# Kernel optimization log

Hardware: AMD Instinct MI355X
Metric: run time of the kernel (lower is better)

The kernel has to match this reference:

```python
import jax, jax.numpy as jnp
import numpy as np

N_NODES = 50000
N_EDGES = 500000
D_NODE = 128
D_EDGE = 128
D_HID = 512
D_OUT = 128


def setup_inputs() -> dict:
    key = jax.random.key(0)
    ks = jax.random.split(key, 6)
    x = jax.random.normal(ks[0], (N_NODES, D_NODE), dtype=jnp.float32)
    edge_index = jax.random.randint(ks[1], (2, N_EDGES), 0, N_NODES, dtype=jnp.int64 if jax.config.jax_enable_x64 else jnp.int32)
    edge_attr = jax.random.normal(ks[2], (N_EDGES, D_EDGE), dtype=jnp.float32)
    cin = 2 * D_NODE + D_EDGE
    W1 = jax.random.normal(ks[3], (cin, D_HID), dtype=jnp.float32) * (1.0 / np.sqrt(cin))
    b1 = jnp.zeros((D_HID,), dtype=jnp.float32)
    W2 = jax.random.normal(ks[4], (D_HID, D_OUT), dtype=jnp.float32) * (1.0 / np.sqrt(D_HID))
    b2 = jnp.zeros((D_OUT,), dtype=jnp.float32)
    return {"x": x, "edge_index": edge_index, "edge_attr": edge_attr,
            "W1": W1, "b1": b1, "W2": W2, "b2": b2}


def reference(x, edge_index, edge_attr, W1, b1, W2, b2):
    row, col = edge_index[0], edge_index[1]
    source = x[row]            # [E, d_node] gather
    target = x[col]            # [E, d_node] gather
    out = jnp.concatenate([source, target, edge_attr], axis=1)  # [E, 2*d_node + d_edge]
    h = jax.nn.relu(out @ W1 + b1)   # [E, d_hid]
    return h @ W2 + b2               # [E, d_out]
```

## Files before the change

kernel.cpp:

```cpp
#include <hip/hip_runtime.h>

#define E_TOTAL 500000
#define DN 128
#define CIN 384
#define DH 512
#define DOUT 128
#define MT 64
#define NBLK 7813
#define LDA 392
#define LDH 520

typedef short short8 __attribute__((ext_vector_type(8)));
typedef float f32x4 __attribute__((ext_vector_type(4)));

__device__ inline short f2bf(float f) {
    unsigned int u = __float_as_uint(f);
    u = (u + 0x7FFFu + ((u >> 16) & 1u)) >> 16;
    return (short)u;
}

__global__ void prep_weights(const float* __restrict__ w1,
                             const float* __restrict__ w2,
                             short* __restrict__ w1t,
                             short* __restrict__ w2t) {
    __shared__ float t[32][33];
    int b = blockIdx.x;
    const float* src; short* dst; int R, C, tr, tc;
    if (b < 192) { src = w1; dst = w1t; R = 384; C = 512; tr = b >> 4; tc = b & 15; }
    else { b -= 192; src = w2; dst = w2t; R = 512; C = 128; tr = b >> 2; tc = b & 3; }
    int lx = threadIdx.x & 31, ly = threadIdx.x >> 5;
#pragma unroll
    for (int p = 0; p < 4; p++) {
        int r = tr * 32 + p * 8 + ly;
        t[p * 8 + ly][lx] = src[(size_t)r * C + tc * 32 + lx];
    }
    __syncthreads();
#pragma unroll
    for (int p = 0; p < 4; p++) {
        int c = tc * 32 + p * 8 + ly;
        dst[(size_t)c * R + tr * 32 + lx] = f2bf(t[lx][p * 8 + ly]);
    }
}

__global__ __launch_bounds__(512, 4) void edge_mlp(
        const float* __restrict__ x,
        const int* __restrict__ ei,
        const float* __restrict__ ea,
        const float* __restrict__ b1,
        const float* __restrict__ b2,
        const short* __restrict__ w1t,
        const short* __restrict__ w2t,
        float* __restrict__ out) {
    __shared__ short sBuf[MT * LDH];
    __shared__ int sIdx[2][MT];
    short (*sA)[LDA] = (short (*)[LDA])sBuf;
    short (*sH)[LDH] = (short (*)[LDH])sBuf;

    const int tid = threadIdx.x;
    const int wave = tid >> 6;
    const int lane = tid & 63;
    const int l16 = lane & 15;
    const int quad = lane >> 4;
    const int e0 = blockIdx.x * MT;

    if (tid < MT) {
        int e = e0 + tid; e = e < E_TOTAL ? e : E_TOTAL - 1;
        sIdx[0][tid] = ei[e];
    } else if (tid < 2 * MT) {
        int r = tid - MT;
        int e = e0 + r; e = e < E_TOTAL ? e : E_TOTAL - 1;
        sIdx[1][r] = ei[E_TOTAL + e];
    }
    __syncthreads();

    {
        const int lane32 = tid & 31;
        const int g = tid >> 5;
        for (int u = g; u < 3 * MT; u += 16) {
            int seg = u >> 6;
            int r = u & 63;
            const float* src;
            if (seg == 0)      src = x + (size_t)sIdx[0][r] * DN;
            else if (seg == 1) src = x + (size_t)sIdx[1][r] * DN;
            else {
                int e = e0 + r; e = e < E_TOTAL ? e : E_TOTAL - 1;
                src = ea + (size_t)e * DN;
            }
            float4 v = reinterpret_cast<const float4*>(src)[lane32];
            short4 p;
            p.x = f2bf(v.x); p.y = f2bf(v.y); p.z = f2bf(v.z); p.w = f2bf(v.w);
            *reinterpret_cast<short4*>(&sA[r][seg * DN + lane32 * 4]) = p;
        }
    }
    __syncthreads();

    f32x4 acc[4][4] = {};
    {
        const int nb = wave * 64;
        const short* base = w1t + (size_t)(nb + l16) * CIN + quad * 8;
        short8 bb[4];
#pragma unroll
        for (int nt = 0; nt < 4; nt++)
            bb[nt] = *reinterpret_cast<const short8*>(base + nt * 16 * CIN);
        for (int k = 0; k < CIN; k += 32) {
            short8 bn[4];
            if (k + 32 < CIN) {
#pragma unroll
                for (int nt = 0; nt < 4; nt++)
                    bn[nt] = *reinterpret_cast<const short8*>(base + nt * 16 * CIN + k + 32);
            }
            short8 a[4];
#pragma unroll
            for (int mt = 0; mt < 4; mt++)
                a[mt] = *reinterpret_cast<const short8*>(&sA[mt * 16 + l16][k + quad * 8]);
#pragma unroll
            for (int nt = 0; nt < 4; nt++)
#pragma unroll
                for (int mt = 0; mt < 4; mt++)
                    acc[mt][nt] = __builtin_amdgcn_mfma_f32_16x16x32_bf16(a[mt], bb[nt], acc[mt][nt], 0, 0, 0);
            if (k + 32 < CIN) {
#pragma unroll
                for (int nt = 0; nt < 4; nt++) bb[nt] = bn[nt];
            }
        }
        __syncthreads();
#pragma unroll
        for (int nt = 0; nt < 4; nt++) {
            int n = nb + nt * 16 + l16;
            float bias = b1[n];
#pragma unroll
            for (int mt = 0; mt < 4; mt++)
#pragma unroll
                for (int r = 0; r < 4; r++) {
                    int m = mt * 16 + quad * 4 + r;
                    sH[m][n] = f2bf(fmaxf(acc[mt][nt][r] + bias, 0.0f));
                }
        }
    }
    __syncthreads();

    {
        f32x4 acc2[4] = {};
        const int n = wave * 16 + l16;
        const short* base2 = w2t + (size_t)n * DH + quad * 8;
        short8 bb = *reinterpret_cast<const short8*>(base2);
        for (int k = 0; k < DH; k += 32) {
            short8 bn;
            if (k + 32 < DH)
                bn = *reinterpret_cast<const short8*>(base2 + k + 32);
            short8 h[4];
#pragma unroll
            for (int mt = 0; mt < 4; mt++)
                h[mt] = *reinterpret_cast<const short8*>(&sH[mt * 16 + l16][k + quad * 8]);
#pragma unroll
            for (int mt = 0; mt < 4; mt++)
                acc2[mt] = __builtin_amdgcn_mfma_f32_16x16x32_bf16(h[mt], bb, acc2[mt], 0, 0, 0);
            if (k + 32 < DH) bb = bn;
        }
        float bias = b2[n];
#pragma unroll
        for (int mt = 0; mt < 4; mt++)
#pragma unroll
            for (int r = 0; r < 4; r++) {
                int m = mt * 16 + quad * 4 + r;
                int e = e0 + m;
                if (e < E_TOTAL)
                    out[(size_t)e * DOUT + n] = acc2[mt][r] + bias;
            }
    }
}

extern "C" void kernel_launch(void* const* d_in, const int* in_sizes, int n_in,
                              void* d_out, int out_size, void* d_ws, size_t ws_size,
                              hipStream_t stream) {
    const float* x  = (const float*)d_in[0];
    const int*   ei = (const int*)d_in[1];
    const float* ea = (const float*)d_in[2];
    const float* W1 = (const float*)d_in[3];
    const float* b1 = (const float*)d_in[4];
    const float* W2 = (const float*)d_in[5];
    const float* b2 = (const float*)d_in[6];
    float* outp = (float*)d_out;

    short* w1t = (short*)d_ws;
    short* w2t = w1t + DH * CIN;

    prep_weights<<<256, 256, 0, stream>>>(W1, W2, w1t, w2t);
    edge_mlp<<<NBLK, 512, 0, stream>>>(x, ei, ea, b1, b2, w1t, w2t, outp);
}
```

Measured before the change: 972.7 us.

## Make edge MLP persistent with software-pipelined gather of next tile

Turns the per-tile grid into 512 persistent blocks that loop over tiles with a stride. The next tile's node and edge features are loaded into registers during the first GEMM epilogue and the second GEMM, and the indices two tiles ahead are prefetched. The MFMA operands are swapped so each lane holds four consecutive columns, which allows vectorized short4 stores to the hidden buffer and float4 output stores. This is meant to hide gather latency behind compute and cut launch overhead, at the cost of more registers per thread and possibly lower occupancy.

```diff
diff --git a/kernel.cpp b/kernel.cpp
--- a/kernel.cpp
+++ b/kernel.cpp
@@ -6,7 +6,8 @@
 #define DH 512
 #define DOUT 128
 #define MT 64
-#define NBLK 7813
+#define NTILE 7813
+#define NPERS 512
 #define LDA 392
 #define LDH 520
 
@@ -52,7 +53,7 @@
         const short* __restrict__ w2t,
         float* __restrict__ out) {
     __shared__ short sBuf[MT * LDH];
-    __shared__ int sIdx[2][MT];
+    __shared__ int sIdx[2][2][MT];
     short (*sA)[LDA] = (short (*)[LDA])sBuf;
     short (*sH)[LDH] = (short (*)[LDH])sBuf;
 
@@ -61,112 +62,172 @@
     const int lane = tid & 63;
     const int l16 = lane & 15;
     const int quad = lane >> 4;
-    const int e0 = blockIdx.x * MT;
-
-    if (tid < MT) {
-        int e = e0 + tid; e = e < E_TOTAL ? e : E_TOTAL - 1;
-        sIdx[0][tid] = ei[e];
-    } else if (tid < 2 * MT) {
-        int r = tid - MT;
-        int e = e0 + r; e = e < E_TOTAL ? e : E_TOTAL - 1;
-        sIdx[1][r] = ei[E_TOTAL + e];
+    const int lane32 = tid & 31;
+    const int g = tid >> 5;
+    const int t0 = blockIdx.x;
+
+    float4 b1v[4];
+#pragma unroll
+    for (int nt = 0; nt < 4; nt++)
+        b1v[nt] = *reinterpret_cast<const float4*>(&b1[wave * 64 + nt * 16 + quad * 4]);
+    float4 b2v = *reinterpret_cast<const float4*>(&b2[wave * 16 + quad * 4]);
+
+    if (tid < 2 * MT) {
+        int rrow = tid >> 6, r = tid & 63;
+        int e = t0 * MT + r; e = e < E_TOTAL ? e : E_TOTAL - 1;
+        sIdx[0][rrow][r] = ei[rrow * E_TOTAL + e];
+        if (t0 + NPERS < NTILE) {
+            int e2 = (t0 + NPERS) * MT + r; e2 = e2 < E_TOTAL ? e2 : E_TOTAL - 1;
+            sIdx[1][rrow][r] = ei[rrow * E_TOTAL + e2];
+        }
     }
     __syncthreads();
-
-    {
-        const int lane32 = tid & 31;
-        const int g = tid >> 5;
-        for (int u = g; u < 3 * MT; u += 16) {
-            int seg = u >> 6;
-            int r = u & 63;
-            const float* src;
-            if (seg == 0)      src = x + (size_t)sIdx[0][r] * DN;
-            else if (seg == 1) src = x + (size_t)sIdx[1][r] * DN;
-            else {
-                int e = e0 + r; e = e < E_TOTAL ? e : E_TOTAL - 1;
-                src = ea + (size_t)e * DN;
-            }
-            float4 v = reinterpret_cast<const float4*>(src)[lane32];
+#pragma unroll
+    for (int j = 0; j < 12; j++) {
+        const int seg = j >> 2;
+        const int r = g + 16 * (j & 3);
+        const float* src;
+        if (seg == 0)      src = x + (size_t)sIdx[0][0][r] * DN;
+        else if (seg == 1) src = x + (size_t)sIdx[0][1][r] * DN;
+        else { int e = t0 * MT + r; e = e < E_TOTAL ? e : E_TOTAL - 1; src = ea + (size_t)e * DN; }
+        float4 v = reinterpret_cast<const float4*>(src)[lane32];
+        short4 p; p.x = f2bf(v.x); p.y = f2bf(v.y); p.z = f2bf(v.z); p.w = f2bf(v.w);
+        *reinterpret_cast<short4*>(&sA[r][seg * DN + lane32 * 4]) = p;
+    }
+    __syncthreads();
+
+#pragma unroll 1
+    for (int i = 0; ; i++) {
+        const int t = t0 + i * NPERS;
+        const int e0 = t * MT;
+        const bool hasN1 = (t + NPERS) < NTILE;
+        const bool hasN2 = (t + 2 * NPERS) < NTILE;
+
+        f32x4 acc[4][4] = {};
+        {
+            const short* base1 = w1t + (size_t)(wave * 64 + l16) * CIN + quad * 8;
+            short8 bb[4];
+#pragma unroll
+            for (int nt = 0; nt < 4; nt++)
+                bb[nt] = *reinterpret_cast<const short8*>(base1 + nt * 16 * CIN);
+            for (int k = 0; k < CIN; k += 32) {
+                short8 bn[4];
+                if (k + 32 < CIN) {
+#pragma unroll
+                    for (int nt = 0; nt < 4; nt++)
+                        bn[nt] = *reinterpret_cast<const short8*>(base1 + nt * 16 * CIN + k + 32);
+                }
+                short8 a[4];
+#pragma unroll
+                for (int mt = 0; mt < 4; mt++)
+                    a[mt] = *reinterpret_cast<const short8*>(&sA[mt * 16 + l16][k + quad * 8]);
+#pragma unroll
+                for (int nt = 0; nt < 4; nt++)
+#pragma unroll
+                    for (int mt = 0; mt < 4; mt++)
+                        acc[nt][mt] = __builtin_amdgcn_mfma_f32_16x16x32_bf16(bb[nt], a[mt], acc[nt][mt], 0, 0, 0);
+                if (k + 32 < CIN) {
+#pragma unroll
+                    for (int nt = 0; nt < 4; nt++) bb[nt] = bn[nt];
+                }
+            }
+        }
+        asm volatile("s_waitcnt lgkmcnt(0)" ::: "memory");
+        __builtin_amdgcn_s_barrier();
+
+#pragma unroll
+        for (int nt = 0; nt < 4; nt++) {
+#pragma unroll
+            for (int mt = 0; mt < 4; mt++) {
+                short4 p;
+                p.x = f2bf(fmaxf(acc[nt][mt][0] + b1v[nt].x, 0.0f));
+                p.y = f2bf(fmaxf(acc[nt][mt][1] + b1v[nt].y, 0.0f));
+                p.z = f2bf(fmaxf(acc[nt][mt][2] + b1v[nt].z, 0.0f));
+                p.w = f2bf(fmaxf(acc[nt][mt][3] + b1v[nt].w, 0.0f));
+                *reinterpret_cast<short4*>(&sH[mt * 16 + l16][wave * 64 + nt * 16 + quad * 4]) = p;
+            }
+        }
+
+        const short* base2 = w2t + (size_t)(wave * 16 + l16) * DH + quad * 8;
+        short8 b2f[4];
+#pragma unroll
+        for (int kk = 0; kk < 4; kk++)
+            b2f[kk] = *reinterpret_cast<const short8*>(base2 + kk * 32);
+
+        float4 gv[12];
+        if (hasN1) {
+            const int* sI0 = sIdx[(i + 1) & 1][0];
+            const int* sI1 = sIdx[(i + 1) & 1][1];
+            const int e0n = (t + NPERS) * MT;
+#pragma unroll
+            for (int j = 0; j < 12; j++) {
+                const int seg = j >> 2;
+                const int r = g + 16 * (j & 3);
+                const float* src;
+                if (seg == 0)      src = x + (size_t)sI0[r] * DN;
+                else if (seg == 1) src = x + (size_t)sI1[r] * DN;
+                else { int e = e0n + r; e = e < E_TOTAL ? e : E_TOTAL - 1; src = ea + (size_t)e * DN; }
+                gv[j] = reinterpret_cast<const float4*>(src)[lane32];
+            }
+        }
+        int idxN = 0;
+        if (hasN2 && tid < 2 * MT) {
+            int rrow = tid >> 6, r = tid & 63;
+            int e2 = (t + 2 * NPERS) * MT + r; e2 = e2 < E_TOTAL ? e2 : E_TOTAL - 1;
+            idxN = ei[rrow * E_TOTAL + e2];
+        }
+        __builtin_amdgcn_sched_barrier(0);
+        asm volatile("s_waitcnt lgkmcnt(0)" ::: "memory");
+        __builtin_amdgcn_s_barrier();
+
+        {
+            f32x4 acc2[4] = {};
+            short8 bw = b2f[0];
+#pragma unroll
+            for (int kk = 0; kk < 16; kk++) {
+                short8 bnext = bw;
+                if (kk < 3) bnext = b2f[kk + 1];
+                else if (kk < 15) bnext = *reinterpret_cast<const short8*>(base2 + (kk + 1) * 32);
+                short8 h[4];
+#pragma unroll
+                for (int mt = 0; mt < 4; mt++)
+                    h[mt] = *reinterpret_cast<const short8*>(&sH[mt * 16 + l16][kk * 32 + quad * 8]);
+#pragma unroll
+                for (int mt = 0; mt < 4; mt++)
+                    acc2[mt] = __builtin_amdgcn_mfma_f32_16x16x32_bf16(bw, h[mt], acc2[mt], 0, 0, 0);
+                bw = bnext;
+            }
+#pragma unroll
+            for (int mt = 0; mt < 4; mt++) {
+                int e = e0 + mt * 16 + l16;
+                if (e < E_TOTAL) {
+                    float4 o;
+                    o.x = acc2[mt][0] + b2v.x;
+                    o.y = acc2[mt][1] + b2v.y;
+                    o.z = acc2[mt][2] + b2v.z;
+                    o.w = acc2[mt][3] + b2v.w;
+                    *reinterpret_cast<float4*>(&out[(size_t)e * DOUT + wave * 16 + quad * 4]) = o;
+                }
+            }
+        }
+
+        if (!hasN1) break;
+
+        asm volatile("s_waitcnt lgkmcnt(0)" ::: "memory");
+        __builtin_amdgcn_s_barrier();
+
+#pragma unroll
+        for (int j = 0; j < 12; j++) {
+            const int seg = j >> 2;
+            const int r = g + 16 * (j & 3);
             short4 p;
-            p.x = f2bf(v.x); p.y = f2bf(v.y); p.z = f2bf(v.z); p.w = f2bf(v.w);
+            p.x = f2bf(gv[j].x); p.y = f2bf(gv[j].y); p.z = f2bf(gv[j].z); p.w = f2bf(gv[j].w);
             *reinterpret_cast<short4*>(&sA[r][seg * DN + lane32 * 4]) = p;
         }
-    }
-    __syncthreads();
-
-    f32x4 acc[4][4] = {};
-    {
-        const int nb = wave * 64;
-        const short* base = w1t + (size_t)(nb + l16) * CIN + quad * 8;
-        short8 bb[4];
-#pragma unroll
-        for (int nt = 0; nt < 4; nt++)
-            bb[nt] = *reinterpret_cast<const short8*>(base + nt * 16 * CIN);
-        for (int k = 0; k < CIN; k += 32) {
-            short8 bn[4];
-            if (k + 32 < CIN) {
-#pragma unroll
-                for (int nt = 0; nt < 4; nt++)
-                    bn[nt] = *reinterpret_cast<const short8*>(base + nt * 16 * CIN + k + 32);
-            }
-            short8 a[4];
-#pragma unroll
-            for (int mt = 0; mt < 4; mt++)
-                a[mt] = *reinterpret_cast<const short8*>(&sA[mt * 16 + l16][k + quad * 8]);
-#pragma unroll
-            for (int nt = 0; nt < 4; nt++)
-#pragma unroll
-                for (int mt = 0; mt < 4; mt++)
-                    acc[mt][nt] = __builtin_amdgcn_mfma_f32_16x16x32_bf16(a[mt], bb[nt], acc[mt][nt], 0, 0, 0);
-            if (k + 32 < CIN) {
-#pragma unroll
-                for (int nt = 0; nt < 4; nt++) bb[nt] = bn[nt];
-            }
-        }
-        __syncthreads();
-#pragma unroll
-        for (int nt = 0; nt < 4; nt++) {
-            int n = nb + nt * 16 + l16;
-            float bias = b1[n];
-#pragma unroll
-            for (int mt = 0; mt < 4; mt++)
-#pragma unroll
-                for (int r = 0; r < 4; r++) {
-                    int m = mt * 16 + quad * 4 + r;
-                    sH[m][n] = f2bf(fmaxf(acc[mt][nt][r] + bias, 0.0f));
-                }
-        }
-    }
-    __syncthreads();
-
-    {
-        f32x4 acc2[4] = {};
-        const int n = wave * 16 + l16;
-        const short* base2 = w2t + (size_t)n * DH + quad * 8;
-        short8 bb = *reinterpret_cast<const short8*>(base2);
-        for (int k = 0; k < DH; k += 32) {
-            short8 bn;
-            if (k + 32 < DH)
-                bn = *reinterpret_cast<const short8*>(base2 + k + 32);
-            short8 h[4];
-#pragma unroll
-            for (int mt = 0; mt < 4; mt++)
-                h[mt] = *reinterpret_cast<const short8*>(&sH[mt * 16 + l16][k + quad * 8]);
-#pragma unroll
-            for (int mt = 0; mt < 4; mt++)
-                acc2[mt] = __builtin_amdgcn_mfma_f32_16x16x32_bf16(h[mt], bb, acc2[mt], 0, 0, 0);
-            if (k + 32 < DH) bb = bn;
-        }
-        float bias = b2[n];
-#pragma unroll
-        for (int mt = 0; mt < 4; mt++)
-#pragma unroll
-            for (int r = 0; r < 4; r++) {
-                int m = mt * 16 + quad * 4 + r;
-                int e = e0 + m;
-                if (e < E_TOTAL)
-                    out[(size_t)e * DOUT + n] = acc2[mt][r] + bias;
-            }
+        if (hasN2 && tid < 2 * MT)
+            sIdx[i & 1][tid >> 6][tid & 63] = idxN;
+        asm volatile("s_waitcnt lgkmcnt(0)" ::: "memory");
+        __builtin_amdgcn_s_barrier();
     }
 }
 
@@ -186,5 +247,5 @@
     short* w2t = w1t + DH * CIN;
 
     prep_weights<<<256, 256, 0, stream>>>(W1, W2, w1t, w2t);
-    edge_mlp<<<NBLK, 512, 0, stream>>>(x, ei, ea, b1, b2, w1t, w2t, outp);
-}
+    edge_mlp<<<NPERS, 512, 0, stream>>>(x, ei, ea, b1, b2, w1t, w2t, outp);
+}
```

Result: slower. 1.487 ms (+52.9%).

## Split fused edge MLP into gather-GEMM1 and GEMM2 kernels with bf16 x

Applied to the files above, without the earlier changes.

Pre-converts node features x to bf16 once so the per-edge gathers read half the bytes, then splits the fused kernel into a gather+GEMM1 kernel that writes the hidden activations to a workspace buffer and a separate GEMM2 kernel, processed in batches sized to fit the workspace. Transposed MFMA operand order allows vectorized bias and output stores. The aim is to cut gather traffic and raise occupancy by giving each kernel a smaller LDS footprint. In exchange it adds a global round trip of the 512-wide bf16 hidden tensor and extra launches, and falls back to the fused kernel if the workspace is too small.

```diff
diff --git a/kernel.cpp b/kernel.cpp
--- a/kernel.cpp
+++ b/kernel.cpp
@@ -1,14 +1,16 @@
 #include <hip/hip_runtime.h>
 
 #define E_TOTAL 500000
+#define N_NODES 50000
 #define DN 128
 #define CIN 384
 #define DH 512
 #define DOUT 128
 #define MT 64
-#define NBLK 7813
+#define NTILE 7813
 #define LDA 392
 #define LDH 520
+#define LDH2 536
 
 typedef short short8 __attribute__((ext_vector_type(8)));
 typedef float f32x4 __attribute__((ext_vector_type(4)));
@@ -39,6 +41,157 @@
     for (int p = 0; p < 4; p++) {
         int c = tc * 32 + p * 8 + ly;
         dst[(size_t)c * R + tr * 32 + lx] = f2bf(t[lx][p * 8 + ly]);
+    }
+}
+
+__global__ void cvt_x(const float* __restrict__ x, short* __restrict__ xb) {
+    int i = blockIdx.x * 256 + threadIdx.x;
+    const float4* s = reinterpret_cast<const float4*>(x) + (size_t)i * 2;
+    float4 a = s[0], b = s[1];
+    short8 p;
+    p[0] = f2bf(a.x); p[1] = f2bf(a.y); p[2] = f2bf(a.z); p[3] = f2bf(a.w);
+    p[4] = f2bf(b.x); p[5] = f2bf(b.y); p[6] = f2bf(b.z); p[7] = f2bf(b.w);
+    reinterpret_cast<short8*>(xb)[i] = p;
+}
+
+__global__ __launch_bounds__(512, 4) void gemm1_gather(
+        const short* __restrict__ xb,
+        const int* __restrict__ ei,
+        const float* __restrict__ ea,
+        const float* __restrict__ b1,
+        const short* __restrict__ w1t,
+        short* __restrict__ h,
+        int e_base) {
+    __shared__ short sA[MT][LDA];
+    __shared__ int sIdx[2][MT];
+    const int tid = threadIdx.x;
+    const int wave = tid >> 6, lane = tid & 63;
+    const int l16 = lane & 15, quad = lane >> 4;
+    const int lane32 = tid & 31, g = tid >> 5;
+    const int e0 = e_base + blockIdx.x * MT;
+
+    if (tid < 2 * MT) {
+        int rr = tid >> 6, r = tid & 63;
+        int e = e0 + r; e = e < E_TOTAL ? e : E_TOTAL - 1;
+        sIdx[rr][r] = ei[rr * E_TOTAL + e];
+    }
+    __syncthreads();
+
+    for (int u = g; u < 3 * MT; u += 16) {
+        int seg = u >> 6, r = u & 63;
+        if (seg < 2) {
+            const short* src = xb + (size_t)sIdx[seg][r] * DN;
+            short4 v = reinterpret_cast<const short4*>(src)[lane32];
+            *reinterpret_cast<short4*>(&sA[r][seg * DN + lane32 * 4]) = v;
+        } else {
+            int e = e0 + r; e = e < E_TOTAL ? e : E_TOTAL - 1;
+            float4 v = reinterpret_cast<const float4*>(ea + (size_t)e * DN)[lane32];
+            short4 p; p.x = f2bf(v.x); p.y = f2bf(v.y); p.z = f2bf(v.z); p.w = f2bf(v.w);
+            *reinterpret_cast<short4*>(&sA[r][2 * DN + lane32 * 4]) = p;
+        }
+    }
+    __syncthreads();
+
+    f32x4 acc[4][4] = {};
+    {
+        const short* base1 = w1t + (size_t)(wave * 64 + l16) * CIN + quad * 8;
+        short8 bb[4];
+#pragma unroll
+        for (int nt = 0; nt < 4; nt++)
+            bb[nt] = *reinterpret_cast<const short8*>(base1 + nt * 16 * CIN);
+        for (int k = 0; k < CIN; k += 32) {
+            short8 bn[4];
+            if (k + 32 < CIN) {
+#pragma unroll
+                for (int nt = 0; nt < 4; nt++)
+                    bn[nt] = *reinterpret_cast<const short8*>(base1 + nt * 16 * CIN + k + 32);
+            }
+            short8 a[4];
+#pragma unroll
+            for (int mt = 0; mt < 4; mt++)
+                a[mt] = *reinterpret_cast<const short8*>(&sA[mt * 16 + l16][k + quad * 8]);
+#pragma unroll
+            for (int nt = 0; nt < 4; nt++)
+#pragma unroll
+                for (int mt = 0; mt < 4; mt++)
+                    acc[nt][mt] = __builtin_amdgcn_mfma_f32_16x16x32_bf16(bb[nt], a[mt], acc[nt][mt], 0, 0, 0);
+            if (k + 32 < CIN) {
+#pragma unroll
+                for (int nt = 0; nt < 4; nt++) bb[nt] = bn[nt];
+            }
+        }
+    }
+    float4 b1v[4];
+#pragma unroll
+    for (int nt = 0; nt < 4; nt++)
+        b1v[nt] = *reinterpret_cast<const float4*>(&b1[wave * 64 + nt * 16 + quad * 4]);
+    short* hb = h + (size_t)blockIdx.x * MT * DH;
+#pragma unroll
+    for (int nt = 0; nt < 4; nt++) {
+#pragma unroll
+        for (int mt = 0; mt < 4; mt++) {
+            short4 p;
+            p.x = f2bf(fmaxf(acc[nt][mt][0] + b1v[nt].x, 0.0f));
+            p.y = f2bf(fmaxf(acc[nt][mt][1] + b1v[nt].y, 0.0f));
+            p.z = f2bf(fmaxf(acc[nt][mt][2] + b1v[nt].z, 0.0f));
+            p.w = f2bf(fmaxf(acc[nt][mt][3] + b1v[nt].w, 0.0f));
+            *reinterpret_cast<short4*>(hb + (size_t)(mt * 16 + l16) * DH
+                                       + wave * 64 + nt * 16 + quad * 4) = p;
+        }
+    }
+}
+
+__global__ __launch_bounds__(512, 4) void gemm2k(
+        const short* __restrict__ h,
+        const float* __restrict__ b2,
+        const short* __restrict__ w2t,
+        float* __restrict__ out,
+        int e_base) {
+    __shared__ short sH[MT][LDH2];
+    const int tid = threadIdx.x;
+    const int wave = tid >> 6, lane = tid & 63;
+    const int l16 = lane & 15, quad = lane >> 4;
+    const int e0 = e_base + blockIdx.x * MT;
+    const short* hb = h + (size_t)blockIdx.x * MT * DH;
+
+    {
+        int r = tid >> 3, c = (tid & 7) * 8;
+#pragma unroll
+        for (int j = 0; j < 8; j++) {
+            short8 v = *reinterpret_cast<const short8*>(hb + (size_t)r * DH + c + j * 64);
+            *reinterpret_cast<short8*>(&sH[r][c + j * 64]) = v;
+        }
+    }
+    __syncthreads();
+
+    f32x4 acc2[4] = {};
+    const short* base2 = w2t + (size_t)(wave * 16 + l16) * DH + quad * 8;
+    short8 bw = *reinterpret_cast<const short8*>(base2);
+#pragma unroll
+    for (int kk = 0; kk < 16; kk++) {
+        short8 bn = bw;
+        if (kk < 15) bn = *reinterpret_cast<const short8*>(base2 + (kk + 1) * 32);
+        short8 hf[4];
+#pragma unroll
+        for (int mt = 0; mt < 4; mt++)
+            hf[mt] = *reinterpret_cast<const short8*>(&sH[mt * 16 + l16][kk * 32 + quad * 8]);
+#pragma unroll
+        for (int mt = 0; mt < 4; mt++)
+            acc2[mt] = __builtin_amdgcn_mfma_f32_16x16x32_bf16(bw, hf[mt], acc2[mt], 0, 0, 0);
+        bw = bn;
+    }
+    float4 b2v = *reinterpret_cast<const float4*>(&b2[wave * 16 + quad * 4]);
+#pragma unroll
+    for (int mt = 0; mt < 4; mt++) {
+        int e = e0 + mt * 16 + l16;
+        if (e < E_TOTAL) {
+            float4 o;
+            o.x = acc2[mt][0] + b2v.x;
+            o.y = acc2[mt][1] + b2v.y;
+            o.z = acc2[mt][2] + b2v.z;
+            o.w = acc2[mt][3] + b2v.w;
+            *reinterpret_cast<float4*>(&out[(size_t)e * DOUT + wave * 16 + quad * 4]) = o;
+        }
     }
 }
 
@@ -55,14 +208,12 @@
     __shared__ int sIdx[2][MT];
     short (*sA)[LDA] = (short (*)[LDA])sBuf;
     short (*sH)[LDH] = (short (*)[LDH])sBuf;
-
     const int tid = threadIdx.x;
     const int wave = tid >> 6;
     const int lane = tid & 63;
     const int l16 = lane & 15;
     const int quad = lane >> 4;
     const int e0 = blockIdx.x * MT;
-
     if (tid < MT) {
         int e = e0 + tid; e = e < E_TOTAL ? e : E_TOTAL - 1;
         sIdx[0][tid] = ei[e];
@@ -72,7 +223,6 @@
         sIdx[1][r] = ei[E_TOTAL + e];
     }
     __syncthreads();
-
     {
         const int lane32 = tid & 31;
         const int g = tid >> 5;
@@ -93,7 +243,6 @@
         }
     }
     __syncthreads();
-
     f32x4 acc[4][4] = {};
     {
         const int nb = wave * 64;
@@ -126,7 +275,7 @@
         __syncthreads();
 #pragma unroll
         for (int nt = 0; nt < 4; nt++) {
-            int n = nb + nt * 16 + l16;
+            int n = wave * 64 + nt * 16 + l16;
             float bias = b1[n];
 #pragma unroll
             for (int mt = 0; mt < 4; mt++)
@@ -138,7 +287,6 @@
         }
     }
     __syncthreads();
-
     {
         f32x4 acc2[4] = {};
         const int n = wave * 16 + l16;
@@ -148,13 +296,13 @@
             short8 bn;
             if (k + 32 < DH)
                 bn = *reinterpret_cast<const short8*>(base2 + k + 32);
-            short8 h[4];
-#pragma unroll
-            for (int mt = 0; mt < 4; mt++)
-                h[mt] = *reinterpret_cast<const short8*>(&sH[mt * 16 + l16][k + quad * 8]);
-#pragma unroll
-            for (int mt = 0; mt < 4; mt++)
-                acc2[mt] = __builtin_amdgcn_mfma_f32_16x16x32_bf16(h[mt], bb, acc2[mt], 0, 0, 0);
+            short8 hh[4];
+#pragma unroll
+            for (int mt = 0; mt < 4; mt++)
+                hh[mt] = *reinterpret_cast<const short8*>(&sH[mt * 16 + l16][k + quad * 8]);
+#pragma unroll
+            for (int mt = 0; mt < 4; mt++)
+                acc2[mt] = __builtin_amdgcn_mfma_f32_16x16x32_bf16(hh[mt], bb, acc2[mt], 0, 0, 0);
             if (k + 32 < DH) bb = bn;
         }
         float bias = b2[n];
@@ -184,7 +332,32 @@
 
     short* w1t = (short*)d_ws;
     short* w2t = w1t + DH * CIN;
-
     prep_weights<<<256, 256, 0, stream>>>(W1, W2, w1t, w2t);
-    edge_mlp<<<NBLK, 512, 0, stream>>>(x, ei, ea, b1, b2, w1t, w2t, outp);
-}
+
+    const size_t base_bytes = (size_t)(DH * CIN + DOUT * DH) * 2;
+    const size_t xb_bytes = (size_t)N_NODES * DN * 2;
+    int nb = 0; size_t tiles_pb = 0;
+    for (int cand = 1; cand <= 8; cand <<= 1) {
+        size_t tpb = (NTILE + cand - 1) / cand;
+        size_t need = base_bytes + xb_bytes + tpb * (size_t)MT * DH * 2;
+        if (need <= ws_size) { nb = cand; tiles_pb = tpb; break; }
+    }
+
+    if (nb == 0) {
+        edge_mlp<<<NTILE, 512, 0, stream>>>(x, ei, ea, b1, b2, w1t, w2t, outp);
+        return;
+    }
+
+    short* xb = w2t + DOUT * DH;
+    short* hbuf = xb + (size_t)N_NODES * DN;
+    cvt_x<<<3125, 256, 0, stream>>>(x, xb);
+
+    int tiles_done = 0;
+    for (int b = 0; b < nb && tiles_done < NTILE; b++) {
+        int tiles = (int)tiles_pb;
+        if (tiles_done + tiles > NTILE) tiles = NTILE - tiles_done;
+        gemm1_gather<<<tiles, 512, 0, stream>>>(xb, ei, ea, b1, w1t, hbuf, tiles_done * MT);
+        gemm2k<<<tiles, 512, 0, stream>>>(hbuf, b2, w2t, outp, tiles_done * MT);
+        tiles_done += tiles;
+    }
+}
```

After: 1.200 ms. 23.4% more time.
